# Kernel tuning notes

Hardware: AMD Instinct MI355X
Metric: run time of the kernel (lower is better)

## Reference

```python
import jax, jax.numpy as jnp
import numpy as np

# ---- module hyperparameters (from init_kwargs / tracker defaults) ----
D_MODEL = 512
D_HEAD = 512
LAMBDA_0 = 1.0        # A_0 = I / lambda_0
FIXED_LAMBDA = 1.0    # fixed penalty magnitude -> U = sqrt(lambda) * K (then / sqrt(d_head))
STAB_EPS = 1e-6       # InversePenaltyTracker.stabilization_eps
PERIODIC_EPS = 1e-6   # InversePenaltyTracker.periodic_eps
PERIOD = 128          # InversePenaltyTracker.period (periodic re-regularization)
EXPLODE_EPS = 1e-5    # fallback_add_explode coefficient
NORM_THRESH = 1000.0  # explosion detection threshold on Frobenius norms


def setup_inputs() -> dict:
    key = jax.random.key(0)
    ks = jax.random.split(key, 9)
    B, T, d = 8, 2048, D_MODEL
    s = 1.0 / np.sqrt(d)
    f32 = jnp.float32
    return {
        "x": jax.random.normal(ks[0], (B, T, d), f32),
        "Wq": (jax.random.normal(ks[1], (D_HEAD, d), f32) * s),
        "bq": jax.random.normal(ks[2], (D_HEAD,), f32) * 0.02,
        "Wk": (jax.random.normal(ks[3], (D_HEAD, d), f32) * s),
        "bk": jax.random.normal(ks[4], (D_HEAD,), f32) * 0.02,
        "Wv": (jax.random.normal(ks[5], (D_HEAD, d), f32) * s),
        "bv": jax.random.normal(ks[6], (D_HEAD,), f32) * 0.02,
        "Wo": (jax.random.normal(ks[7], (d, D_HEAD), f32) * s),
        "bo": jax.random.normal(ks[8], (d,), f32) * 0.02,
    }


def _vla_forward(x, Wq, bq, Wk, bk, Wv, bv, Wo, bo):
    B, T, _ = x.shape
    d = D_HEAD
    # projections (nn.Linear: x @ W.T + b)
    Q = jnp.einsum('btd,hd->bth', x, Wq) + bq
    K = jnp.einsum('btd,hd->bth', x, Wk) + bk
    V = jnp.einsum('btd,hd->bth', x, Wv) + bv

    # PenaltyBuilder (rank 1, fixed lambda): u_t = sqrt(lambda) * k_t, then / sqrt(d_head)
    U = (jnp.sqrt(jnp.float32(FIXED_LAMBDA)) / jnp.sqrt(jnp.float32(d))) * K
    s_seq = jnp.sum(K * Q, axis=-1)                                   # (B,T)
    Vn = V / (jnp.linalg.norm(V, axis=-1, keepdims=True) + 1e-6)      # (B,T,d)

    I = jnp.eye(d, dtype=jnp.float32)
    A0 = jnp.zeros((B, d, d), jnp.float32) + I / LAMBDA_0
    S0 = jnp.zeros((B, d, d), jnp.float32)

    def step(carry, inp):
        A, S = carry
        q, u, s_t, vn, t = inp  # q,u,vn: (B,d); s_t: (B,); t: scalar int
        # Sherman-Morrison rank-1 inverse update with stabilization
        z = jnp.einsum('bij,bj->bi', A, u)
        dot = jnp.sum(u * z, axis=-1)
        delta = jnp.maximum(1.0 + dot, 1e-6)
        unstable = (jnp.abs(delta) < STAB_EPS) | ~jnp.isfinite(delta)
        safe = jnp.where(unstable, 1.0, delta)
        upd = (z[:, :, None] * z[:, None, :]) / safe[:, None, None]
        A = jnp.where(unstable[:, None, None], A + STAB_EPS * I, A - upd)
        # periodic re-regularization (inv_step = t+1)
        A = jnp.where(((t + 1) % PERIOD) == 0, A + PERIODIC_EPS * I, A)
        # alpha_t = s_t * (A u_t)
        z2 = jnp.einsum('bij,bj->bi', A, u)
        alpha = s_t[:, None] * z2
        # memory update S += v_norm alpha^T
        S = S + vn[:, :, None] * alpha[:, None, :]
        # explosion guard
        Sn = jnp.linalg.norm(S.reshape(S.shape[0], -1), axis=-1)
        An = jnp.linalg.norm(A.reshape(A.shape[0], -1), axis=-1)
        A = jnp.where(((Sn > NORM_THRESH) | (An > NORM_THRESH))[:, None, None],
                      A + EXPLODE_EPS * I, A)
        o = jnp.einsum('bij,bj->bi', S, q)
        return (A, S), o

    xs = (jnp.swapaxes(Q, 0, 1), jnp.swapaxes(U, 0, 1),
          jnp.swapaxes(s_seq, 0, 1), jnp.swapaxes(Vn, 0, 1),
          jnp.arange(T))
    _, O = jax.lax.scan(step, (A0, S0), xs)    # O: (T,B,d)
    O = jnp.swapaxes(O, 0, 1)                  # (B,T,d)
    return jnp.einsum('bth,dh->btd', O, Wo) + bo


def reference(x, Wq, bq, Wk, bk, Wv, bv, Wo, bo):
    return _vla_forward(x, Wq, bq, Wk, bk, Wv, bv, Wo, bo)
```

## Files before the change

### kernel.cpp

```cpp
#include <hip/hip_runtime.h>
#include <hip/hip_bf16.h>

#define BB 8
#define TT 2048
#define DD 512
#define LL 128
#define NC 16
#define ETH 512

typedef unsigned short u16;
typedef unsigned int u32;
typedef __attribute__((ext_vector_type(8))) short bf16x8v;
typedef __attribute__((ext_vector_type(4))) float f32x4v;

__device__ __forceinline__ float bf2f(u32 h) { return __uint_as_float(h << 16); }
__device__ __forceinline__ u16 f2bf(float f) {
    u32 u = __float_as_uint(f);
    u += 0x7fffu + ((u >> 16) & 1u);
    return (u16)(u >> 16);
}
__device__ __forceinline__ float wred64(float v) {
    #pragma unroll
    for (int off = 32; off; off >>= 1) v += __shfl_xor(v, off);
    return v;
// ... 113 lines not shown
                        af[mf][ks], bfr[nf][ks], acc[mf][nf], 0, 0, 0);
    }
    const int l15 = lane & 15, lhi = lane >> 4;
    #pragma unroll
    for (int mf = 0; mf < 4; ++mf) {
        #pragma unroll
        for (int nf = 0; nf < 4; ++nf) {
            const int n = n0 + wn * 64 + nf * 16 + l15;
            const float bsv = bias[n];
            #pragma unroll
            for (int r = 0; r < 4; ++r) {
                const int m = m0 + wm * 64 + mf * 16 + lhi * 4 + r;
                const float val = (acc[mf][nf][r] + bsv) * outscale;
                if (OUT_BF) ((u16*)Cout)[(size_t)m * 512 + n] = f2bf(val);
                else        ((float*)Cout)[(size_t)m * 512 + n] = val;
            }
        }
    }
}

__device__ __forceinline__ void mfk6_body(const u16* __restrict__ Sb,
    const u16* __restrict__ Qt, const u16* __restrict__ AlT,
    const u16* __restrict__ Vnt, float* __restrict__ OBSA,
    float* __restrict__ dsum, const int bz)
{
    __shared__ u16 Ah[128 * 64];
    __shared__ u16 Bh[128 * 64];
    const int tid = threadIdx.x, wave = tid >> 6, lane = tid & 63;
    const int wm = wave >> 1, wn = wave & 1;
    const int m0 = blockIdx.x * 128, n0 = blockIdx.y * 128;

    f32x4v acc[4][4];
    #pragma unroll
    for (int i = 0; i < 4; ++i)
        #pragma unroll
        for (int j = 0; j < 4; ++j)
            acc[i][j] = (f32x4v){0.f, 0.f, 0.f, 0.f};

    const u16* Abase = Sb + (size_t)bz * 262144;
    const u16* Bbase = (n0 == 0) ? (Qt + (size_t)bz * 1048576)
                                 : (AlT + (size_t)bz * 65536);
    const u16* gA[4]; const u16* gB[4];
    #pragma unroll
    for (int i = 0; i < 4; ++i) {
        const int idx = i * 256 + tid, row = idx >> 3, c = idx & 7;
        const int kb = c ^ (row & 7);
        gA[i] = Abase + (size_t)(m0 + row) * 512 + kb * 8;
        gB[i] = Bbase + (size_t)row * 512 + kb * 8;
    }
    for (int k0 = 0; k0 < 512; k0 += 64) {
        __syncthreads();
        #pragma unroll
        for (int i = 0; i < 4; ++i) {
// ... 51 lines not shown
            }
        }
    if (n0 == 128) {
        const u16* Vn = Vnt + (size_t)bz * 1048576;
        #pragma unroll
        for (int nf = 0; nf < 4; ++nf) {
            const int n = n0 + wn * 64 + nf * 16 + l15;
            const int i2 = n - 128;
            float part = 0.f;
            #pragma unroll
            for (int mf = 0; mf < 4; ++mf) {
                const int m = m0 + wm * 64 + mf * 16 + lhi * 4;
                const ushort4 vr = *(const ushort4*)(Vn + (size_t)i2 * 512 + m);
                part += bf2f(vr.x) * acc[mf][nf][0] + bf2f(vr.y) * acc[mf][nf][1]
                      + bf2f(vr.z) * acc[mf][nf][2] + bf2f(vr.w) * acc[mf][nf][3];
            }
            part += __shfl_xor(part, 16);
            part += __shfl_xor(part, 32);
            if (lhi == 0) atomicAdd(dsum + bz * 128 + i2, part);
        }
    }
}

__global__ __launch_bounds__(256)
void mfk1_kernel(const u16* __restrict__ Abf, const u16* __restrict__ Ut,
                 float* __restrict__ Wm)
{
    __shared__ u16 Ah[128 * 64];
    __shared__ u16 Bh[128 * 64];
    const int tid = threadIdx.x, wave = tid >> 6, lane = tid & 63;
    const int wm = wave >> 1, wn = wave & 1;
    const int m0 = blockIdx.x * 128;
    const int bz = blockIdx.z;

    f32x4v acc[4][4];
    #pragma unroll
    for (int i = 0; i < 4; ++i)
        #pragma unroll
        for (int j = 0; j < 4; ++j)
            acc[i][j] = (f32x4v){0.f, 0.f, 0.f, 0.f};

    const u16* Abase = Abf + (size_t)bz * 262144;
    const u16* Bbase = Ut + (size_t)bz * 1048576;
    const u16* gA[4]; const u16* gB[4];
    #pragma unroll
    for (int i = 0; i < 4; ++i) {
        const int idx = i * 256 + tid, row = idx >> 3, c = idx & 7;
        const int kb = c ^ (row & 7);
        gA[i] = Abase + (size_t)(m0 + row) * 512 + kb * 8;
        gB[i] = Bbase + (size_t)row * 512 + kb * 8;
    }
    for (int k0 = 0; k0 < 512; k0 += 64) {
        __syncthreads();
        #pragma unroll
        for (int i = 0; i < 4; ++i) {
            const int dst = (i * 256 + wave * 64) * 8;
            __builtin_amdgcn_global_load_lds(
                (__attribute__((address_space(1))) void*)(gA[i] + k0),
                (__attribute__((address_space(3))) void*)(Ah + dst), 16, 0, 0);
            __builtin_amdgcn_global_load_lds(
                (__attribute__((address_space(1))) void*)(gB[i] + k0),
                (__attribute__((address_space(3))) void*)(Bh + dst), 16, 0, 0);
        }
        asm volatile("s_waitcnt vmcnt(0)" ::: "memory");
        __syncthreads();

        const int l15 = lane & 15, lhi = lane >> 4;
        bf16x8v af[4][2], bfr[4][2];
        #pragma unroll
        for (int mf = 0; mf < 4; ++mf) {
            const int row = wm * 64 + mf * 16 + l15, sw = (row & 7) << 4;
            #pragma unroll
            for (int ks = 0; ks < 2; ++ks) {
                const int kb2 = (ks * 64 + lhi * 16) ^ sw;
                af[mf][ks] = *(const bf16x8v*)((const char*)Ah + row * 128 + kb2);
            }
        }
        #pragma unroll
        for (int nf = 0; nf < 4; ++nf) {
            const int row = wn * 64 + nf * 16 + l15, sw = (row & 7) << 4;
            #pragma unroll
            for (int ks = 0; ks < 2; ++ks) {
                const int kb2 = (ks * 64 + lhi * 16) ^ sw;
                bfr[nf][ks] = *(const bf16x8v*)((const char*)Bh + row * 128 + kb2);
            }
        }
        #pragma unroll
        for (int ks = 0; ks < 2; ++ks)
            #pragma unroll
            for (int mf = 0; mf < 4; ++mf)
                #pragma unroll
                for (int nf = 0; nf < 4; ++nf)
                    acc[mf][nf] = __builtin_amdgcn_mfma_f32_16x16x32_bf16(
                        af[mf][ks], bfr[nf][ks], acc[mf][nf], 0, 0, 0);
    }
    const int l15 = lane & 15, lhi = lane >> 4;
    float* C = Wm + (size_t)bz * 65536;
    #pragma unroll
    for (int mf = 0; mf < 4; ++mf)
        #pragma unroll
        for (int nf = 0; nf < 4; ++nf) {
            const int n = wn * 64 + nf * 16 + l15;
            #pragma unroll
            for (int r = 0; r < 4; ++r) {
                const int m = m0 + wm * 64 + mf * 16 + lhi * 4 + r;
                C[(size_t)m * 128 + n] = acc[mf][nf][r];
            }
        }
}

__global__ __launch_bounds__(256)
void prep_kernel(const u16* __restrict__ Qb, const u16* __restrict__ Ub,
                 u16* __restrict__ Vb, float* __restrict__ sseq)
{
    const int lane = threadIdx.x & 63, wid = threadIdx.x >> 6;
    const int row = blockIdx.x * 4 + wid;
    const size_t base = (size_t)row * DD;
    const uint4 qr = *(const uint4*)(Qb + base + lane * 8);
    const uint4 ur = *(const uint4*)(Ub + base + lane * 8);
    const uint4 vr = *(const uint4*)(Vb + base + lane * 8);
    float q[8], u[8], v[8];
    unpack8(qr, q); unpack8(ur, u); unpack8(vr, v);
    float sd = 0.f, nv = 0.f;
    #pragma unroll
    for (int e = 0; e < 8; ++e) { sd = fmaf(q[e], u[e], sd); nv = fmaf(v[e], v[e], nv); }
    #pragma unroll
    for (int off = 32; off; off >>= 1) { sd += __shfl_xor(sd, off); nv += __shfl_xor(nv, off); }
    if (lane == 0) sseq[row] = sd * 22.627416997969522f;
    const float inv = 1.f / (sqrtf(nv) + 1e-6f);
    uint4 o;
    o.x = (u32)f2bf(v[0] * inv) | ((u32)f2bf(v[1] * inv) << 16);
// ... 15 lines not shown
        const int e0 = idx << 2;
        const int r = (e0 >> 9) & 511;
        const int c = e0 & 511;
        float4 v;
        v.x = (c + 0 == r) ? 1.f : 0.f;
        v.y = (c + 1 == r) ? 1.f : 0.f;
        v.z = (c + 2 == r) ? 1.f : 0.f;
        v.w = (c + 3 == r) ? 1.f : 0.f;
        A4[idx] = v;
        S4[idx] = make_float4(0.f, 0.f, 0.f, 0.f);
        Sbf4[idx] = z4;
        if (Abf4) {
            ushort4 a;
            a.x = (c + 0 == r) ? 0x3F80 : 0;
            a.y = (c + 1 == r) ? 0x3F80 : 0;
            a.z = (c + 2 == r) ? 0x3F80 : 0;
            a.w = (c + 3 == r) ? 0x3F80 : 0;
            Abf4[idx] = a;
        }
    }
    if (gtid < BB) { SnSq[gtid] = 0.f; AnAcc[gtid] = 512.f; }
}

struct GP {
    int alay, blay, epi;
    const void* Ap; const void* Bp;
    void* Cp; float* Cio;
    const float* gdiag; float* anacc;
    const float* invdp; const float* cap; const float* cbp;
    const u16* Ulastp; float* Zsp; float* Alphap;
    u16* albt; u16* sbf; u16* abf;
    int lda, ldb, ldc, K;
    long sA, sB, sC, sCio;
};

__device__ __forceinline__ void gemm_body(const GP& p, const int bz) {
    __shared__ __align__(16) float As[32][68];
    __shared__ __align__(16) float Bs[32][68];
    const int m0 = blockIdx.x * 64, n0 = blockIdx.y * 64;
    const int tid = threadIdx.x, tx = tid & 15, ty = tid >> 4;
    float acc[4][4] = {};
    for (int k0 = 0; k0 < p.K; k0 += 32) {
        if (p.alay == 0) {
            const float* A = (const float*)p.Ap + (size_t)bz * p.sA;
            #pragma unroll
            for (int h = 0; h < 2; ++h) {
// ... 135 lines not shown
            const int n = nb + j;
            const float iv = p.invdp[bz * 128 + n];
            const float cav = p.cap[bz * 128 + n];
            const float cbv = p.cbp[bz * 128 + n];
            #pragma unroll
            for (int i = 0; i < 4; ++i) {
                const int m = mb + i;
                const float z = acc[i][j];
                const size_t o = (size_t)m * 128 + n;
                Zb[o] = z;
                Zsb[o] = z * iv;
                float a = z * cav;
                if (cbv != 0.f) a = fmaf(cbv, bf2f(p.Ulastp[(size_t)bz * 1048576 + m]), a);
                Apb[o] = a;
                p.albt[(size_t)bz * 65536 + (size_t)n * 512 + m] = f2bf(a);
            }
        }
    }
}

__global__ __launch_bounds__(256) void gemmx(GP p) { gemm_body(p, blockIdx.z); }

__global__ __launch_bounds__(256)
void lvl5_kernel(const u16* Sb, const u16* AlT, const float* Alpha,
                 const u16* Qt, const u16* Vnt,
                 float* P, float* Ga, float* Gv, float* OBSA, float* dsum)
{
    const int z = blockIdx.z;
    if (z < 8) {
        mfk6_body(Sb, Qt, AlT, Vnt, OBSA, dsum, z);
        return;
    }
    if (blockIdx.x >= 2 || blockIdx.y >= 2) return;
    const int zz = z - 8, b = zz / 3, j = zz - b * 3;
    GP p{};
    p.K = 512; p.epi = 0; p.ldc = 128; p.sC = 16384;
    if (j == 0) {
        p.alay = 1; p.Ap = Alpha; p.lda = 128; p.sA = 65536;
        p.blay = 3; p.Bp = Qt; p.ldb = 512; p.sB = 1048576; p.Cp = P;
    } else if (j == 1) {
        p.alay = 1; p.Ap = Alpha; p.lda = 128; p.sA = 65536;
        p.blay = 0; p.Bp = Alpha; p.ldb = 128; p.sB = 65536; p.Cp = Ga;
    } else {
        p.alay = 2; p.Ap = Vnt; p.lda = 512; p.sA = 1048576;
        p.blay = 3; p.Bp = Vnt; p.ldb = 512; p.sB = 1048576; p.Cp = Gv;
    }
    gemm_body(p, b);
}

__global__ __launch_bounds__(256)
void lvl7_kernel(const float* P, const u16* Vnt, u16* Obt, const float* OBSA,
                 const float* Alpha, const float* Zs, const float* Z,
                 float* S, u16* Sbf, float* A, u16* Abf,
                 const float* gdiag, float* AnAcc)
{
    const int z = blockIdx.z;
    GP p{};
    if (z < 8) {
        p.alay = 0; p.Ap = Zs; p.lda = 128; p.sA = 65536;
        p.blay = 1; p.Bp = Z; p.ldb = 128; p.sB = 65536;
        p.epi = 1; p.Cio = A; p.sCio = 262144; p.ldc = 512;
        p.gdiag = gdiag; p.anacc = AnAcc; p.abf = Abf; p.K = 128;
        gemm_body(p, z);
    } else if (z < 16) {
        p.alay = 3; p.Ap = Vnt; p.lda = 512; p.sA = 1048576;
        p.blay = 1; p.Bp = Alpha; p.ldb = 128; p.sB = 65536;
        p.epi = 2; p.Cio = S; p.sbf = Sbf; p.sCio = 262144; p.ldc = 512; p.K = 128;
        gemm_body(p, z - 8);
    } else {
        if (blockIdx.x >= 2) return;
        p.alay = 4; p.Ap = P; p.lda = 128; p.sA = 16384;
        p.blay = 2; p.Bp = Vnt; p.ldb = 512; p.sB = 1048576;
        p.epi = 3; p.Cp = Obt; p.ldc = 512; p.sC = 1048576;
        p.Cio = (float*)OBSA; p.sCio = 131072; p.K = 128;
        gemm_body(p, z - 16);
    }
}

__global__ __launch_bounds__(512)
void elim_kernel(const float* __restrict__ G, float* __restrict__ Tg,
                 const float* __restrict__ sseq, float* __restrict__ invd,
                 float* __restrict__ ca, float* __restrict__ cb,
                 float* __restrict__ dsum_g, const int t0)
{
    const int b = blockIdx.x, tid = threadIdx.x, lane = tid & 63, wave = tid >> 6;
    __shared__ __align__(16) float E[128][132];
    __shared__ __align__(16) float Cs[128][132];
    __shared__ __align__(16) float Scr[2368];
    __shared__ float del[128];
    float (*Tm)[132] = E;
    float (*LpT)[132] = (float(*)[132])Scr;
    float (*SpT)[132] = (float(*)[132])(Scr + 1056);

    {
        const float4* Gb = (const float4*)(G + (size_t)b * 16384);
        for (int idx = tid; idx < 4096; idx += ETH) {
            const int r = idx >> 5, c4 = idx & 31;
            ((float4*)&E[r][0])[c4] = Gb[idx];
        }
    }
    if (tid < 128) dsum_g[b * 128 + tid] = 0.f;
    __syncthreads();

    for (int p = 0; p < 16; ++p) {
        const int pc0 = p * 8;
        if (wave == 0) {
            float pr0[8], pr1[8];
            #pragma unroll
            for (int j = 0; j < 8; ++j) {
                pr0[j] = E[pc0 + j][lane];
                pr1[j] = E[pc0 + j][64 + lane];
            }
            float dl[8];
            const bool hi = (pc0 >= 64);
            #pragma unroll
            for (int j = 0; j < 8; ++j) {
                const int t = pc0 + j;
                const int pl = t & 63;
                float prow[8];
                #pragma unroll
                for (int c = 0; c < 8; ++c) {
                    const float v0 = __shfl(pr0[c], pl);
                    const float v1 = __shfl(pr1[c], pl);
                    prow[c] = hi ? v1 : v0;
                }
                const float d = fmaxf(1.f + prow[j], 1e-6f);
                dl[j] = d;
                const float inv = 1.f / d;
                if (lane > t) {
                    const float coef = pr0[j] * inv;
                    #pragma unroll
                    for (int c = j + 1; c < 8; ++c) pr0[c] = fmaf(-coef, prow[c], pr0[c]);
                }
                if (lane + 64 > t) {
                    const float coef = pr1[j] * inv;
                    #pragma unroll
                    for (int c = j + 1; c < 8; ++c) pr1[c] = fmaf(-coef, prow[c], pr1[c]);
                }
            }
            #pragma unroll
            for (int j = 0; j < 8; ++j) {
                const float idj = 1.f / dl[j];
                const int t = pc0 + j;
                {
                    const bool below = (lane > t);
                    const float y = below ? pr0[j] : 0.f;
                    const float l = y * idj;
                    LpT[j][lane] = l; SpT[j][lane] = y; Cs[t][lane] = l;
                }
                {
                    const int r = lane + 64;
                    const bool below = (r > t);
                    const float y = below ? pr1[j] : 0.f;
                    const float l = y * idj;
                    LpT[j][r] = l; SpT[j][r] = y; Cs[t][r] = l;
                }
            }
            if (lane < 8) del[pc0 + lane] = dl[lane];
        }
        __syncthreads();
        const int r0b = pc0 + 8;
        if (r0b < 128) {
            const int nrows = 128 - r0b;
            const int c40 = r0b >> 2, nc4 = 32 - c40;
            for (int idx = tid; idx < nrows * nc4; idx += ETH) {
                const int rr = idx / nc4, cc = idx - rr * nc4;
                const int r = r0b + rr, c4 = c40 + cc;
                float4 e = ((float4*)&E[r][0])[c4];
                #pragma unroll
                for (int j = 0; j < 8; ++j) {
                    const float lv = LpT[j][r];
                    const float4 sv = ((const float4*)&SpT[j][0])[c4];
                    e.x = fmaf(-lv, sv.x, e.x);
                    e.y = fmaf(-lv, sv.y, e.y);
                    e.z = fmaf(-lv, sv.z, e.z);
                    e.w = fmaf(-lv, sv.w, e.w);
                }
                ((float4*)&E[r][0])[c4] = e;
            }
        }
        __syncthreads();
    }

    for (int idx = tid; idx < 4224; idx += ETH)
        ((float4*)&Tm[0][0])[idx] = make_float4(0.f, 0.f, 0.f, 0.f);
    __syncthreads();
    if (tid < 128) Tm[tid][tid] = 1.f;
    __syncthreads();
    {
        const int g = tid >> 3, c = tid & 7;
        if (g < 16) {
            for (int r2 = c - 1; r2 >= 0; --r2) {
                float s = 0.f;
                for (int kk = r2 + 1; kk <= c; ++kk)
                    s = fmaf(Cs[8 * g + r2][8 * g + kk],
                             (kk == c) ? 1.f : Tm[8 * g + kk][8 * g + c], s);
                Tm[8 * g + r2][8 * g + c] = -s;
            }
        }
    }
    __syncthreads();
    for (int s = 8; s <= 64; s <<= 1) {
        const int npairs = 64 / s;
        const int nj = (s == 64) ? 32 : s;
        const int stride = nj + 4;
        const int nj4 = nj >> 2;
        const int Nel = npairs * s * nj4;
        const int nhalf = (s == 64) ? 2 : 1;
        for (int jh = 0; jh < nhalf; ++jh) {
            for (int idx = tid; idx < Nel; idx += ETH) {
                const int p2 = idx / (s * nj4), rem = idx - p2 * s * nj4;
                const int i = rem / nj4, j4 = rem - i * nj4;
                const int I0 = 2 * s * p2, J0 = I0 + s;
                const int jc = j4 * 4 + jh * 32;
                float4 x = make_float4(0.f, 0.f, 0.f, 0.f);
                for (int k = 0; k < s; ++k) {
                    const float cv = Cs[I0 + i][J0 + k];
                    const float4 tv = *(const float4*)&Tm[J0 + k][J0 + jc];
                    x.x = fmaf(cv, tv.x, x.x);
                    x.y = fmaf(cv, tv.y, x.y);
                    x.z = fmaf(cv, tv.z, x.z);
                    x.w = fmaf(cv, tv.w, x.w);
                }
                *(float4*)&Scr[p2 * s * stride + i * stride + j4 * 4] = x;
            }
            __syncthreads();
            for (int idx = tid; idx < Nel; idx += ETH) {
                const int p2 = idx / (s * nj4), rem = idx - p2 * s * nj4;
                const int i = rem / nj4, j4 = rem - i * nj4;
                const int I0 = 2 * s * p2, J0 = I0 + s;
                const int jc = j4 * 4 + jh * 32;
                float4 y = make_float4(0.f, 0.f, 0.f, 0.f);
                for (int k = 0; k < s; ++k) {
                    const float tv = Tm[I0 + i][I0 + k];
                    const float4 xv = *(const float4*)&Scr[p2 * s * stride + k * stride + j4 * 4];
                    y.x = fmaf(tv, xv.x, y.x);
                    y.y = fmaf(tv, xv.y, y.y);
                    y.z = fmaf(tv, xv.z, y.z);
                    y.w = fmaf(tv, xv.w, y.w);
                }
                float4 o;
                o.x = -y.x; o.y = -y.y; o.z = -y.z; o.w = -y.w;
                *(float4*)&Tm[I0 + i][J0 + jc] = o;
            }
            __syncthreads();
        }
    }
    {
        float4* Tgb = (float4*)(Tg + (size_t)b * 16384);
        for (int idx = tid; idx < 4096; idx += ETH) {
            const int r = idx >> 5, c4 = idx & 31;
            Tgb[idx] = ((const float4*)&Tm[r][0])[c4];
        }
    }
    if (tid < 128) {
        const float d = del[tid];
        const float s = sseq[(size_t)b * TT + t0 + tid];
        invd[b * 128 + tid] = 1.f / d;
        ca[b * 128 + tid] = s / d;
        cb[b * 128 + tid] = (tid == 127) ? s * 1e-6f : 0.f;
    }
}

__global__ __launch_bounds__(256)
void guard_kernel(const float* __restrict__ dsum_g, const float* __restrict__ Ga,
                  const float* __restrict__ Gv, float* __restrict__ SnSq,
                  float* __restrict__ AnAcc, float* __restrict__ gdiag)
{
    const int b = blockIdx.x, tid = threadIdx.x;
    __shared__ float rpart[256], dsh[128], mdia[128];
    const int t = tid & 127, half = tid >> 7;
    const float* gv = Gv + (size_t)b * 16384 + t * 128;
    const float* ga = Ga + (size_t)b * 16384 + t * 128;
    float rs = 0.f;
    for (int j = half; j < t; j += 2) rs = fmaf(gv[j], ga[j], rs);
    rpart[tid] = rs;
    if (half == 0) { dsh[t] = dsum_g[b * 128 + t]; mdia[t] = gv[t] * ga[t]; }
    __syncthreads();
    if (tid == 0) {
        const float An2 = AnAcc[b];
        float Sn2 = SnSq[b], D = 0.f, T = 0.f;
        int ng = 0;
        for (int t2 = 0; t2 < 128; ++t2) {
// ... 37 lines not shown
    float* OBSA = (float*)(ws + (88ull << 20));
    float* G    = (float*)(ws + (92ull << 20));
    float* Tg   = (float*)(ws + (92ull << 20) + (512ull << 10));
    float* P    = (float*)(ws + (93ull << 20));
    float* Ga   = (float*)(ws + (93ull << 20) + (512ull << 10));
    float* Gv   = (float*)(ws + (94ull << 20));
    float* invd = (float*)(ws + (94ull << 20) + (512ull << 10));
    float* ca   = (float*)(ws + (94ull << 20) + (516ull << 10));
    float* cb   = (float*)(ws + (94ull << 20) + (520ull << 10));
    float* sseq = (float*)(ws + (94ull << 20) + (528ull << 10));
    float* SnSq = (float*)(ws + (94ull << 20) + (600ull << 10));
    float* AnAcc= (float*)(ws + (94ull << 20) + (600ull << 10) + 64);
    float* gdiag= (float*)(ws + (94ull << 20) + (600ull << 10) + 128);
    float* dsum = (float*)(ws + (94ull << 20) + (604ull << 10));
    u16* Wq_bf = (u16*)(ws + (95ull << 20));
    u16* Wk_bf = (u16*)(ws + (95ull << 20) + (512ull << 10));
    u16* Wv_bf = (u16*)(ws + (96ull << 20));
    u16* Wo_bf = (u16*)(ws + (96ull << 20) + (512ull << 10));
    u16* S_bf  = (u16*)(ws + (97ull << 20));
    u16* AlT   = (u16*)(ws + (101ull << 20));

    const bool big = (ws_size >= (111ull << 20));
    u16* A_bf = big ? (u16*)(ws + (102ull << 20)) : (u16*)nullptr;

    f2bf_kernel<<<2048, 256, 0, stream>>>((const float4*)x, (ushort4*)x_bf, 2097152);
    wconv_kernel<<<dim3(256, 4), 256, 0, stream>>>(
        (const float4*)Wq, (const float4*)Wk, (const float4*)Wv, (const float4*)Wo,
        (ushort4*)Wq_bf, (ushort4*)Wk_bf, (ushort4*)Wv_bf, (ushort4*)Wo_bf);

    mfma_gemm<1><<<dim3(128, 4), 256, 0, stream>>>(x_bf, Wq_bf, bq, Qb, 1.f);
    mfma_gemm<1><<<dim3(128, 4), 256, 0, stream>>>(x_bf, Wk_bf, bk, Ub, 0.04419417382415922f);
    mfma_gemm<1><<<dim3(128, 4), 256, 0, stream>>>(x_bf, Wv_bf, bv, Vnb, 1.f);
    prep_kernel<<<4096, 256, 0, stream>>>(Qb, Ub, Vnb, sseq);
    init_kernel<<<2048, 256, 0, stream>>>((float4*)A, (float4*)S, (ushort4*)S_bf,
                                          (ushort4*)A_bf, SnSq, AnAcc);

    for (int c = 0; c < NC; ++c) {
        const int t0 = c * LL;
        const u16* Ut = Ub + (size_t)t0 * 512;
        const u16* Qt = Qb + (size_t)t0 * 512;
        const u16* Vt = Vnb + (size_t)t0 * 512;
        if (big) {
            mfk1_kernel<<<dim3(4, 1, 8), 256, 0, stream>>>(A_bf, Ut, Wm);
        } else {
            GP p1{}; p1.alay = 0; p1.Ap = A; p1.lda = 512; p1.sA = 262144;
            p1.blay = 3; p1.Bp = Ut; p1.ldb = 512; p1.sB = 1048576;
            p1.epi = 0; p1.Cp = Wm; p1.ldc = 128; p1.sC = 65536; p1.K = 512;
            gemmx<<<dim3(8, 2, 8), 256, 0, stream>>>(p1);
        }
        GP p2{}; p2.alay = 2; p2.Ap = Ut; p2.lda = 512; p2.sA = 1048576;
        p2.blay = 0; p2.Bp = Wm; p2.ldb = 128; p2.sB = 65536;
        p2.epi = 0; p2.Cp = G; p2.ldc = 128; p2.sC = 16384; p2.K = 512;
        gemmx<<<dim3(2, 2, 8), 256, 0, stream>>>(p2);
        elim_kernel<<<8, 512, 0, stream>>>(G, Tg, sseq, invd, ca, cb, dsum, t0);
        GP p4{}; p4.alay = 0; p4.Ap = Wm; p4.lda = 128; p4.sA = 65536;
        p4.blay = 0; p4.Bp = Tg; p4.ldb = 128; p4.sB = 16384;
        p4.epi = 4; p4.Cp = Z; p4.Zsp = Zs; p4.Alphap = Alpha; p4.albt = AlT;
        p4.invdp = invd; p4.cap = ca; p4.cbp = cb;
        p4.Ulastp = Ub + (size_t)(t0 + 127) * 512;
        p4.K = 128; p4.ldc = 128; p4.sC = 65536;
        gemmx<<<dim3(8, 2, 8), 256, 0, stream>>>(p4);
        lvl5_kernel<<<dim3(4, 2, 32), 256, 0, stream>>>(S_bf, AlT, Alpha, Qt, Vt,
            P, Ga, Gv, OBSA, dsum);
        guard_kernel<<<8, 256, 0, stream>>>(dsum, Ga, Gv, SnSq, AnAcc, gdiag);
        lvl7_kernel<<<dim3(8, 8, 24), 256, 0, stream>>>(P, Vt, Ob + (size_t)t0 * 512, OBSA,
            Alpha, Zs, Z, S, S_bf, A, A_bf, gdiag, AnAcc);
    }
    mfma_gemm<0><<<dim3(128, 4), 256, 0, stream>>>(Ob, Wo_bf, bo, d_out, 1.f);
}
```

Before: 3.366 ms.

## Split elimination kernel and co-schedule independent S·Q and Vn Gram work

The monolithic per-batch elimination kernel is split into an LDL factor stage and a separate triangular-inverse kernel. The factor stage is packed into one launch together with work that does not depend on it: the S·Q product (mfk6q8 body) and the Vn Gram matrix (gv512), previously done in the later lvl5 launch, are moved earlier. This lets the serial 8-block factorization share the GPU with other blocks and shrinks lvl5's grid. The cost is an extra launch per chunk, a global round trip for the factor matrix, and many idle blocks that exit early in the combined grid.

```diff
diff --git a/kernel.cpp b/kernel.cpp
--- a/kernel.cpp
+++ b/kernel.cpp
@@ -159,13 +159,12 @@
 __device__ __forceinline__ void mfk6_body(const u16* __restrict__ Sb,
     const u16* __restrict__ Qt, const u16* __restrict__ AlT,
     const u16* __restrict__ Vnt, float* __restrict__ OBSA,
-    float* __restrict__ dsum, const int bz)
+    float* __restrict__ dsum, const int m0, const int n0, const int bz)
 {
     __shared__ u16 Ah[128 * 64];
     __shared__ u16 Bh[128 * 64];
     const int tid = threadIdx.x, wave = tid >> 6, lane = tid & 63;
     const int wm = wave >> 1, wn = wave & 1;
-    const int m0 = blockIdx.x * 128, n0 = blockIdx.y * 128;
 
     f32x4v acc[4][4];
     #pragma unroll
@@ -263,30 +262,29 @@
     }
 }
 
-__global__ __launch_bounds__(256)
-void mfk1_kernel(const u16* __restrict__ Abf, const u16* __restrict__ Ut,
-                 float* __restrict__ Wm)
-{
-    __shared__ u16 Ah[128 * 64];
-    __shared__ u16 Bh[128 * 64];
+__device__ __forceinline__ void mfk6q8_body(char* smemc,
+    const u16* __restrict__ Sb, const u16* __restrict__ Qt,
+    float* __restrict__ OBSA, const int bz)
+{
+    u16* Ah = (u16*)smemc;
+    u16* Bh = (u16*)(smemc + 16384);
     const int tid = threadIdx.x, wave = tid >> 6, lane = tid & 63;
     const int wm = wave >> 1, wn = wave & 1;
     const int m0 = blockIdx.x * 128;
-    const int bz = blockIdx.z;
-
-    f32x4v acc[4][4];
-    #pragma unroll
-    for (int i = 0; i < 4; ++i)
+
+    f32x4v acc[2][4];
+    #pragma unroll
+    for (int i = 0; i < 2; ++i)
         #pragma unroll
         for (int j = 0; j < 4; ++j)
             acc[i][j] = (f32x4v){0.f, 0.f, 0.f, 0.f};
 
-    const u16* Abase = Abf + (size_t)bz * 262144;
-    const u16* Bbase = Ut + (size_t)bz * 1048576;
-    const u16* gA[4]; const u16* gB[4];
-    #pragma unroll
-    for (int i = 0; i < 4; ++i) {
-        const int idx = i * 256 + tid, row = idx >> 3, c = idx & 7;
+    const u16* Abase = Sb + (size_t)bz * 262144;
+    const u16* Bbase = Qt + (size_t)bz * 1048576;
+    const u16* gA[2]; const u16* gB[2];
+    #pragma unroll
+    for (int i = 0; i < 2; ++i) {
+        const int idx = i * 512 + tid, row = idx >> 3, c = idx & 7;
         const int kb = c ^ (row & 7);
         gA[i] = Abase + (size_t)(m0 + row) * 512 + kb * 8;
         gB[i] = Bbase + (size_t)row * 512 + kb * 8;
@@ -294,8 +292,8 @@
     for (int k0 = 0; k0 < 512; k0 += 64) {
         __syncthreads();
         #pragma unroll
-        for (int i = 0; i < 4; ++i) {
-            const int dst = (i * 256 + wave * 64) * 8;
+        for (int i = 0; i < 2; ++i) {
+            const int dst = (i * 512 + wave * 64) * 8;
             __builtin_amdgcn_global_load_lds(
                 (__attribute__((address_space(1))) void*)(gA[i] + k0),
                 (__attribute__((address_space(3))) void*)(Ah + dst), 16, 0, 0);
@@ -307,10 +305,10 @@
         __syncthreads();
 
         const int l15 = lane & 15, lhi = lane >> 4;
-        bf16x8v af[4][2], bfr[4][2];
-        #pragma unroll
-        for (int mf = 0; mf < 4; ++mf) {
-            const int row = wm * 64 + mf * 16 + l15, sw = (row & 7) << 4;
+        bf16x8v af[2][2], bfr[4][2];
+        #pragma unroll
+        for (int mf = 0; mf < 2; ++mf) {
+            const int row = wm * 32 + mf * 16 + l15, sw = (row & 7) << 4;
             #pragma unroll
             for (int ks = 0; ks < 2; ++ks) {
                 const int kb2 = (ks * 64 + lhi * 16) ^ sw;
@@ -329,25 +327,282 @@
         #pragma unroll
         for (int ks = 0; ks < 2; ++ks)
             #pragma unroll
-            for (int mf = 0; mf < 4; ++mf)
+            for (int mf = 0; mf < 2; ++mf)
                 #pragma unroll
                 for (int nf = 0; nf < 4; ++nf)
                     acc[mf][nf] = __builtin_amdgcn_mfma_f32_16x16x32_bf16(
                         af[mf][ks], bfr[nf][ks], acc[mf][nf], 0, 0, 0);
     }
     const int l15 = lane & 15, lhi = lane >> 4;
-    float* C = Wm + (size_t)bz * 65536;
-    #pragma unroll
-    for (int mf = 0; mf < 4; ++mf)
+    float* C = OBSA + (size_t)bz * 131072;
+    #pragma unroll
+    for (int mf = 0; mf < 2; ++mf)
         #pragma unroll
         for (int nf = 0; nf < 4; ++nf) {
             const int n = wn * 64 + nf * 16 + l15;
             #pragma unroll
             for (int r = 0; r < 4; ++r) {
-                const int m = m0 + wm * 64 + mf * 16 + lhi * 4 + r;
-                C[(size_t)m * 128 + n] = acc[mf][nf][r];
-            }
-        }
+                const int m = m0 + wm * 32 + mf * 16 + lhi * 4 + r;
+                C[(size_t)m * 256 + n] = acc[mf][nf][r];
+            }
+        }
+}
+
+__device__ __forceinline__ void gv512_body(char* smemc, const u16* __restrict__ Vnt,
+    float* __restrict__ Gv, const int b)
+{
+    float (*As)[68] = (float(*)[68])smemc;
+    float (*Bs)[68] = (float(*)[68])(smemc + 8704);
+    const int tid = threadIdx.x;
+    const int m0 = blockIdx.x * 64, n0 = blockIdx.y * 64;
+    const u16* Vn = Vnt + (size_t)b * 1048576;
+    const int tx = tid & 15, ty = tid >> 4;
+    float acc[2][4] = {};
+    for (int k0 = 0; k0 < 512; k0 += 32) {
+        const int m = tid >> 3, k4 = (tid & 7) * 4;
+        const ushort4 ra = *(const ushort4*)(Vn + (size_t)(m0 + m) * 512 + k0 + k4);
+        As[k4][m]=bf2f(ra.x); As[k4+1][m]=bf2f(ra.y); As[k4+2][m]=bf2f(ra.z); As[k4+3][m]=bf2f(ra.w);
+        const ushort4 rb = *(const ushort4*)(Vn + (size_t)(n0 + m) * 512 + k0 + k4);
+        Bs[k4][m]=bf2f(rb.x); Bs[k4+1][m]=bf2f(rb.y); Bs[k4+2][m]=bf2f(rb.z); Bs[k4+3][m]=bf2f(rb.w);
+        __syncthreads();
+        #pragma unroll
+        for (int kk = 0; kk < 32; ++kk) {
+            const float a0 = As[kk][ty * 2], a1 = As[kk][ty * 2 + 1];
+            const float4 bv = *(const float4*)&Bs[kk][tx * 4];
+            acc[0][0] = fmaf(a0, bv.x, acc[0][0]);
+            acc[0][1] = fmaf(a0, bv.y, acc[0][1]);
+            acc[0][2] = fmaf(a0, bv.z, acc[0][2]);
+            acc[0][3] = fmaf(a0, bv.w, acc[0][3]);
+            acc[1][0] = fmaf(a1, bv.x, acc[1][0]);
+            acc[1][1] = fmaf(a1, bv.y, acc[1][1]);
+            acc[1][2] = fmaf(a1, bv.z, acc[1][2]);
+            acc[1][3] = fmaf(a1, bv.w, acc[1][3]);
+        }
+        __syncthreads();
+    }
+    float* G = Gv + (size_t)b * 16384;
+    #pragma unroll
+    for (int i = 0; i < 2; ++i)
+        #pragma unroll
+        for (int j = 0; j < 4; ++j)
+            G[(size_t)(m0 + ty * 2 + i) * 128 + n0 + tx * 4 + j] = acc[i][j];
+}
+
+__device__ __forceinline__ void factor_body(char* smemc,
+    const float* __restrict__ G, float* __restrict__ Cg,
+    const float* __restrict__ sseq, float* __restrict__ invd,
+    float* __restrict__ ca, float* __restrict__ cb, const int t0, const int b)
+{
+    const int tid = threadIdx.x, lane = tid & 63, wave = tid >> 6;
+    float (*E)[132]   = (float(*)[132])smemc;
+    float (*LpT)[132] = (float(*)[132])(smemc + 67584);
+    float (*SpT)[132] = (float(*)[132])(smemc + 71808);
+    float* del        = (float*)(smemc + 76032);
+
+    {
+        const float4* Gb = (const float4*)(G + (size_t)b * 16384);
+        for (int idx = tid; idx < 4096; idx += ETH) {
+            const int r = idx >> 5, c4 = idx & 31;
+            ((float4*)&E[r][0])[c4] = Gb[idx];
+        }
+    }
+    __syncthreads();
+    float* Cb = Cg + (size_t)b * 16384;
+
+    for (int p = 0; p < 16; ++p) {
+        const int pc0 = p * 8;
+        if (wave == 0) {
+            float pr0[8], pr1[8];
+            #pragma unroll
+            for (int j = 0; j < 8; ++j) {
+                pr0[j] = E[pc0 + j][lane];
+                pr1[j] = E[pc0 + j][64 + lane];
+            }
+            float dl[8];
+            const bool hi = (pc0 >= 64);
+            #pragma unroll
+            for (int j = 0; j < 8; ++j) {
+                const int t = pc0 + j;
+                const int pl = t & 63;
+                float prow[8];
+                if (hi) {
+                    #pragma unroll
+                    for (int c = 0; c < 8; ++c) prow[c] = __shfl(pr1[c], pl);
+                } else {
+                    #pragma unroll
+                    for (int c = 0; c < 8; ++c) prow[c] = __shfl(pr0[c], pl);
+                }
+                const float d = fmaxf(1.f + prow[j], 1e-6f);
+                dl[j] = d;
+                const float inv = 1.f / d;
+                if (lane > t) {
+                    const float coef = pr0[j] * inv;
+                    #pragma unroll
+                    for (int c = j + 1; c < 8; ++c) pr0[c] = fmaf(-coef, prow[c], pr0[c]);
+                }
+                if (lane + 64 > t) {
+                    const float coef = pr1[j] * inv;
+                    #pragma unroll
+                    for (int c = j + 1; c < 8; ++c) pr1[c] = fmaf(-coef, prow[c], pr1[c]);
+                }
+            }
+            #pragma unroll
+            for (int j = 0; j < 8; ++j) {
+                const float idj = 1.f / dl[j];
+                const int t = pc0 + j;
+                {
+                    const bool below = (lane > t);
+                    const float y = below ? pr0[j] : 0.f;
+                    const float l = y * idj;
+                    LpT[j][lane] = l; SpT[j][lane] = y;
+                    Cb[(size_t)t * 128 + lane] = l;
+                }
+                {
+                    const int r = lane + 64;
+                    const bool below = (r > t);
+                    const float y = below ? pr1[j] : 0.f;
+                    const float l = y * idj;
+                    LpT[j][r] = l; SpT[j][r] = y;
+                    Cb[(size_t)t * 128 + r] = l;
+                }
+            }
+            if (lane < 8) del[pc0 + lane] = dl[lane];
+        }
+        __syncthreads();
+        const int r0b = pc0 + 8;
+        if (r0b < 128) {
+            const int nrows = 128 - r0b;
+            const int c40 = r0b >> 2, nc4 = 32 - c40;
+            for (int idx = tid; idx < nrows * nc4; idx += ETH) {
+                const int rr = idx / nc4, cc = idx - rr * nc4;
+                const int r = r0b + rr, c4 = c40 + cc;
+                float4 e = ((float4*)&E[r][0])[c4];
+                #pragma unroll
+                for (int j = 0; j < 8; ++j) {
+                    const float lv = LpT[j][r];
+                    const float4 sv = ((const float4*)&SpT[j][0])[c4];
+                    e.x = fmaf(-lv, sv.x, e.x);
+                    e.y = fmaf(-lv, sv.y, e.y);
+                    e.z = fmaf(-lv, sv.z, e.z);
+                    e.w = fmaf(-lv, sv.w, e.w);
+                }
+                ((float4*)&E[r][0])[c4] = e;
+            }
+        }
+        __syncthreads();
+    }
+    if (tid < 128) {
+        const float d = del[tid];
+        const float s = sseq[(size_t)b * TT + t0 + tid];
+        invd[b * 128 + tid] = 1.f / d;
+        ca[b * 128 + tid] = s / d;
+        cb[b * 128 + tid] = (tid == 127) ? s * 1e-6f : 0.f;
+    }
+}
+
+__global__ __launch_bounds__(512)
+void lvl3_kernel(const float* __restrict__ G, float* __restrict__ Cg,
+                 const float* __restrict__ sseq, float* __restrict__ invd,
+                 float* __restrict__ ca, float* __restrict__ cb,
+                 const u16* __restrict__ Vnt, const u16* __restrict__ Sb,
+                 const u16* __restrict__ Qt, float* __restrict__ Gv,
+                 float* __restrict__ OBSA, const int t0)
+{
+    __shared__ __align__(16) char smem[76800];
+    const int z = blockIdx.z;
+    if (z >= 16) {
+        if (blockIdx.y != 0) return;
+        mfk6q8_body(smem, Sb, Qt, OBSA, z - 16);
+        return;
+    }
+    if (z >= 8) {
+        if (blockIdx.x >= 2 || blockIdx.y >= 2) return;
+        gv512_body(smem, Vnt, Gv, z - 8);
+        return;
+    }
+    if (blockIdx.x != 0 || blockIdx.y != 0) return;
+    factor_body(smem, G, Cg, sseq, invd, ca, cb, t0, z);
+}
+
+__global__ __launch_bounds__(512)
+void inv_kernel(const float* __restrict__ Cg, float* __restrict__ Tg)
+{
+    const int b = blockIdx.x, tid = threadIdx.x;
+    __shared__ __align__(16) float Tm[128][132];
+    __shared__ __align__(16) float Scr[2368];
+    const float* Cb = Cg + (size_t)b * 16384;
+
+    for (int idx = tid; idx < 4224; idx += ETH)
+        ((float4*)&Tm[0][0])[idx] = make_float4(0.f, 0.f, 0.f, 0.f);
+    __syncthreads();
+    if (tid < 128) Tm[tid][tid] = 1.f;
+    __syncthreads();
+    {
+        const int g = tid >> 3, c = tid & 7;
+        if (g < 16) {
+            for (int r2 = c - 1; r2 >= 0; --r2) {
+                float s = 0.f;
+                for (int kk = r2 + 1; kk <= c; ++kk)
+                    s = fmaf(Cb[(size_t)(8 * g + r2) * 128 + 8 * g + kk],
+                             (kk == c) ? 1.f : Tm[8 * g + kk][8 * g + c], s);
+                Tm[8 * g + r2][8 * g + c] = -s;
+            }
+        }
+    }
+    __syncthreads();
+    for (int s = 8; s <= 64; s <<= 1) {
+        const int npairs = 64 / s;
+        const int nj = (s == 64) ? 32 : s;
+        const int stride = nj + 4;
+        const int nj4 = nj >> 2;
+        const int Nel = npairs * s * nj4;
+        const int nhalf = (s == 64) ? 2 : 1;
+        for (int jh = 0; jh < nhalf; ++jh) {
+            for (int idx = tid; idx < Nel; idx += ETH) {
+                const int p2 = idx / (s * nj4), rem = idx - p2 * s * nj4;
+                const int i = rem / nj4, j4 = rem - i * nj4;
+                const int I0 = 2 * s * p2, J0 = I0 + s;
+                const int jc = j4 * 4 + jh * 32;
+                float4 x = make_float4(0.f, 0.f, 0.f, 0.f);
+                for (int k = 0; k < s; ++k) {
+                    const float cv = Cb[(size_t)(I0 + i) * 128 + J0 + k];
+                    const float4 tv = *(const float4*)&Tm[J0 + k][J0 + jc];
+                    x.x = fmaf(cv, tv.x, x.x);
+                    x.y = fmaf(cv, tv.y, x.y);
+                    x.z = fmaf(cv, tv.z, x.z);
+                    x.w = fmaf(cv, tv.w, x.w);
+                }
+                *(float4*)&Scr[p2 * s * stride + i * stride + j4 * 4] = x;
+            }
+            __syncthreads();
+            for (int idx = tid; idx < Nel; idx += ETH) {
+                const int p2 = idx / (s * nj4), rem = idx - p2 * s * nj4;
+                const int i = rem / nj4, j4 = rem - i * nj4;
+                const int I0 = 2 * s * p2, J0 = I0 + s;
+                const int jc = j4 * 4 + jh * 32;
+                float4 y = make_float4(0.f, 0.f, 0.f, 0.f);
+                for (int k = 0; k < s; ++k) {
+                    const float tv = Tm[I0 + i][I0 + k];
+                    const float4 xv = *(const float4*)&Scr[p2 * s * stride + k * stride + j4 * 4];
+                    y.x = fmaf(tv, xv.x, y.x);
+                    y.y = fmaf(tv, xv.y, y.y);
+                    y.z = fmaf(tv, xv.z, y.z);
+                    y.w = fmaf(tv, xv.w, y.w);
+                }
+                float4 o;
+                o.x = -y.x; o.y = -y.y; o.z = -y.z; o.w = -y.w;
+                *(float4*)&Tm[I0 + i][J0 + jc] = o;
+            }
+            __syncthreads();
+        }
+    }
+    {
+        float4* Tgb = (float4*)(Tg + (size_t)b * 16384);
+        for (int idx = tid; idx < 4096; idx += ETH) {
+            const int r = idx >> 5, c4 = idx & 31;
+            Tgb[idx] = ((const float4*)&Tm[r][0])[c4];
+        }
+    }
 }
 
 __global__ __launch_bounds__(256)
@@ -409,6 +664,93 @@
     if (gtid < BB) { SnSq[gtid] = 0.f; AnAcc[gtid] = 512.f; }
 }
 
+__global__ __launch_bounds__(256)
+void mfk1_kernel(const u16* __restrict__ Abf, const u16* __restrict__ Ut,
+                 float* __restrict__ Wm)
+{
+    __shared__ u16 Ah[128 * 64];
+    __shared__ u16 Bh[128 * 64];
+    const int tid = threadIdx.x, wave = tid >> 6, lane = tid & 63;
+    const int wm = wave >> 1, wn = wave & 1;
+    const int m0 = blockIdx.x * 128;
+    const int bz = blockIdx.z;
+
+    f32x4v acc[4][4];
+    #pragma unroll
+    for (int i = 0; i < 4; ++i)
+        #pragma unroll
+        for (int j = 0; j < 4; ++j)
+            acc[i][j] = (f32x4v){0.f, 0.f, 0.f, 0.f};
+
+    const u16* Abase = Abf + (size_t)bz * 262144;
+    const u16* Bbase = Ut + (size_t)bz * 1048576;
+    const u16* gA[4]; const u16* gB[4];
+    #pragma unroll
+    for (int i = 0; i < 4; ++i) {
+        const int idx = i * 256 + tid, row = idx >> 3, c = idx & 7;
+        const int kb = c ^ (row & 7);
+        gA[i] = Abase + (size_t)(m0 + row) * 512 + kb * 8;
+        gB[i] = Bbase + (size_t)row * 512 + kb * 8;
+    }
+    for (int k0 = 0; k0 < 512; k0 += 64) {
+        __syncthreads();
+        #pragma unroll
+        for (int i = 0; i < 4; ++i) {
+            const int dst = (i * 256 + wave * 64) * 8;
+            __builtin_amdgcn_global_load_lds(
+                (__attribute__((address_space(1))) void*)(gA[i] + k0),
+                (__attribute__((address_space(3))) void*)(Ah + dst), 16, 0, 0);
+            __builtin_amdgcn_global_load_lds(
+                (__attribute__((address_space(1))) void*)(gB[i] + k0),
+                (__attribute__((address_space(3))) void*)(Bh + dst), 16, 0, 0);
+        }
+        asm volatile("s_waitcnt vmcnt(0)" ::: "memory");
+        __syncthreads();
+
+        const int l15 = lane & 15, lhi = lane >> 4;
+        bf16x8v af[4][2], bfr[4][2];
+        #pragma unroll
+        for (int mf = 0; mf < 4; ++mf) {
+            const int row = wm * 64 + mf * 16 + l15, sw = (row & 7) << 4;
+            #pragma unroll
+            for (int ks = 0; ks < 2; ++ks) {
+                const int kb2 = (ks * 64 + lhi * 16) ^ sw;
+                af[mf][ks] = *(const bf16x8v*)((const char*)Ah + row * 128 + kb2);
+            }
+        }
+        #pragma unroll
+        for (int nf = 0; nf < 4; ++nf) {
+            const int row = wn * 64 + nf * 16 + l15, sw = (row & 7) << 4;
+            #pragma unroll
+            for (int ks = 0; ks < 2; ++ks) {
+                const int kb2 = (ks * 64 + lhi * 16) ^ sw;
+                bfr[nf][ks] = *(const bf16x8v*)((const char*)Bh + row * 128 + kb2);
+            }
+        }
+        #pragma unroll
+        for (int ks = 0; ks < 2; ++ks)
+            #pragma unroll
+            for (int mf = 0; mf < 4; ++mf)
+                #pragma unroll
+                for (int nf = 0; nf < 4; ++nf)
+                    acc[mf][nf] = __builtin_amdgcn_mfma_f32_16x16x32_bf16(
+                        af[mf][ks], bfr[nf][ks], acc[mf][nf], 0, 0, 0);
+    }
+    const int l15 = lane & 15, lhi = lane >> 4;
+    float* C = Wm + (size_t)bz * 65536;
+    #pragma unroll
+    for (int mf = 0; mf < 4; ++mf)
+        #pragma unroll
+        for (int nf = 0; nf < 4; ++nf) {
+            const int n = wn * 64 + nf * 16 + l15;
+            #pragma unroll
+            for (int r = 0; r < 4; ++r) {
+                const int m = m0 + wm * 64 + mf * 16 + lhi * 4 + r;
+                C[(size_t)m * 128 + n] = acc[mf][nf][r];
+            }
+        }
+}
+
 struct GP {
     int alay, blay, epi;
     const void* Ap; const void* Bp;
@@ -590,30 +932,36 @@
 __global__ __launch_bounds__(256) void gemmx(GP p) { gemm_body(p, blockIdx.z); }
 
 __global__ __launch_bounds__(256)
-void lvl5_kernel(const u16* Sb, const u16* AlT, const float* Alpha,
-                 const u16* Qt, const u16* Vnt,
-                 float* P, float* Ga, float* Gv, float* OBSA, float* dsum)
+void k2_kernel(GP p, float* __restrict__ dsum)
+{
+    if (blockIdx.x == 0 && blockIdx.y == 0 && threadIdx.x < 128)
+        dsum[blockIdx.z * 128 + threadIdx.x] = 0.f;
+    gemm_body(p, blockIdx.z);
+}
+
+__global__ __launch_bounds__(256)
+void lvl5c_kernel(const u16* Sb, const u16* AlT, const float* Alpha,
+                  const u16* Qt, const u16* Vnt,
+                  float* P, float* Ga, float* OBSA, float* dsum)
 {
     const int z = blockIdx.z;
     if (z < 8) {
-        mfk6_body(Sb, Qt, AlT, Vnt, OBSA, dsum, z);
+        if (blockIdx.y != 0) return;
+        mfk6_body(Sb, Qt, AlT, Vnt, OBSA, dsum, blockIdx.x * 128, 128, z);
         return;
     }
     if (blockIdx.x >= 2 || blockIdx.y >= 2) return;
-    const int zz = z - 8, b = zz / 3, j = zz - b * 3;
     GP p{};
     p.K = 512; p.epi = 0; p.ldc = 128; p.sC = 16384;
-    if (j == 0) {
+    if (z < 16) {
         p.alay = 1; p.Ap = Alpha; p.lda = 128; p.sA = 65536;
         p.blay = 3; p.Bp = Qt; p.ldb = 512; p.sB = 1048576; p.Cp = P;
-    } else if (j == 1) {
+        gemm_body(p, z - 8);
+    } else {
         p.alay = 1; p.Ap = Alpha; p.lda = 128; p.sA = 65536;
         p.blay = 0; p.Bp = Alpha; p.ldb = 128; p.sB = 65536; p.Cp = Ga;
-    } else {
-        p.alay = 2; p.Ap = Vnt; p.lda = 512; p.sA = 1048576;
-        p.blay = 3; p.Bp = Vnt; p.ldb = 512; p.sB = 1048576; p.Cp = Gv;
-    }
-    gemm_body(p, b);
+        gemm_body(p, z - 16);
+    }
 }
 
 __global__ __launch_bounds__(256)
@@ -642,191 +990,6 @@
         p.epi = 3; p.Cp = Obt; p.ldc = 512; p.sC = 1048576;
         p.Cio = (float*)OBSA; p.sCio = 131072; p.K = 128;
         gemm_body(p, z - 16);
-    }
-}
-
-__global__ __launch_bounds__(512)
-void elim_kernel(const float* __restrict__ G, float* __restrict__ Tg,
-                 const float* __restrict__ sseq, float* __restrict__ invd,
-                 float* __restrict__ ca, float* __restrict__ cb,
-                 float* __restrict__ dsum_g, const int t0)
-{
-    const int b = blockIdx.x, tid = threadIdx.x, lane = tid & 63, wave = tid >> 6;
-    __shared__ __align__(16) float E[128][132];
-    __shared__ __align__(16) float Cs[128][132];
-    __shared__ __align__(16) float Scr[2368];
-    __shared__ float del[128];
-    float (*Tm)[132] = E;
-    float (*LpT)[132] = (float(*)[132])Scr;
-    float (*SpT)[132] = (float(*)[132])(Scr + 1056);
-
-    {
-        const float4* Gb = (const float4*)(G + (size_t)b * 16384);
-        for (int idx = tid; idx < 4096; idx += ETH) {
-            const int r = idx >> 5, c4 = idx & 31;
-            ((float4*)&E[r][0])[c4] = Gb[idx];
-        }
-    }
-    if (tid < 128) dsum_g[b * 128 + tid] = 0.f;
-    __syncthreads();
-
-    for (int p = 0; p < 16; ++p) {
-        const int pc0 = p * 8;
-        if (wave == 0) {
-            float pr0[8], pr1[8];
-            #pragma unroll
-            for (int j = 0; j < 8; ++j) {
-                pr0[j] = E[pc0 + j][lane];
-                pr1[j] = E[pc0 + j][64 + lane];
-            }
-            float dl[8];
-            const bool hi = (pc0 >= 64);
-            #pragma unroll
-            for (int j = 0; j < 8; ++j) {
-                const int t = pc0 + j;
-                const int pl = t & 63;
-                float prow[8];
-                #pragma unroll
-                for (int c = 0; c < 8; ++c) {
-                    const float v0 = __shfl(pr0[c], pl);
-                    const float v1 = __shfl(pr1[c], pl);
-                    prow[c] = hi ? v1 : v0;
-                }
-                const float d = fmaxf(1.f + prow[j], 1e-6f);
-                dl[j] = d;
-                const float inv = 1.f / d;
-                if (lane > t) {
-                    const float coef = pr0[j] * inv;
-                    #pragma unroll
-                    for (int c = j + 1; c < 8; ++c) pr0[c] = fmaf(-coef, prow[c], pr0[c]);
-                }
-                if (lane + 64 > t) {
-                    const float coef = pr1[j] * inv;
-                    #pragma unroll
-                    for (int c = j + 1; c < 8; ++c) pr1[c] = fmaf(-coef, prow[c], pr1[c]);
-                }
-            }
-            #pragma unroll
-            for (int j = 0; j < 8; ++j) {
-                const float idj = 1.f / dl[j];
-                const int t = pc0 + j;
-                {
-                    const bool below = (lane > t);
-                    const float y = below ? pr0[j] : 0.f;
-                    const float l = y * idj;
-                    LpT[j][lane] = l; SpT[j][lane] = y; Cs[t][lane] = l;
-                }
-                {
-                    const int r = lane + 64;
-                    const bool below = (r > t);
-                    const float y = below ? pr1[j] : 0.f;
-                    const float l = y * idj;
-                    LpT[j][r] = l; SpT[j][r] = y; Cs[t][r] = l;
-                }
-            }
-            if (lane < 8) del[pc0 + lane] = dl[lane];
-        }
-        __syncthreads();
-        const int r0b = pc0 + 8;
-        if (r0b < 128) {
-            const int nrows = 128 - r0b;
-            const int c40 = r0b >> 2, nc4 = 32 - c40;
-            for (int idx = tid; idx < nrows * nc4; idx += ETH) {
-                const int rr = idx / nc4, cc = idx - rr * nc4;
-                const int r = r0b + rr, c4 = c40 + cc;
-                float4 e = ((float4*)&E[r][0])[c4];
-                #pragma unroll
-                for (int j = 0; j < 8; ++j) {
-                    const float lv = LpT[j][r];
-                    const float4 sv = ((const float4*)&SpT[j][0])[c4];
-                    e.x = fmaf(-lv, sv.x, e.x);
-                    e.y = fmaf(-lv, sv.y, e.y);
-                    e.z = fmaf(-lv, sv.z, e.z);
-                    e.w = fmaf(-lv, sv.w, e.w);
-                }
-                ((float4*)&E[r][0])[c4] = e;
-            }
-        }
-        __syncthreads();
-    }
-
-    for (int idx = tid; idx < 4224; idx += ETH)
-        ((float4*)&Tm[0][0])[idx] = make_float4(0.f, 0.f, 0.f, 0.f);
-    __syncthreads();
-    if (tid < 128) Tm[tid][tid] = 1.f;
-    __syncthreads();
-    {
-        const int g = tid >> 3, c = tid & 7;
-        if (g < 16) {
-            for (int r2 = c - 1; r2 >= 0; --r2) {
-                float s = 0.f;
-                for (int kk = r2 + 1; kk <= c; ++kk)
-                    s = fmaf(Cs[8 * g + r2][8 * g + kk],
-                             (kk == c) ? 1.f : Tm[8 * g + kk][8 * g + c], s);
-                Tm[8 * g + r2][8 * g + c] = -s;
-            }
-        }
-    }
-    __syncthreads();
-    for (int s = 8; s <= 64; s <<= 1) {
-        const int npairs = 64 / s;
-        const int nj = (s == 64) ? 32 : s;
-        const int stride = nj + 4;
-        const int nj4 = nj >> 2;
-        const int Nel = npairs * s * nj4;
-        const int nhalf = (s == 64) ? 2 : 1;
-        for (int jh = 0; jh < nhalf; ++jh) {
-            for (int idx = tid; idx < Nel; idx += ETH) {
-                const int p2 = idx / (s * nj4), rem = idx - p2 * s * nj4;
-                const int i = rem / nj4, j4 = rem - i * nj4;
-                const int I0 = 2 * s * p2, J0 = I0 + s;
-                const int jc = j4 * 4 + jh * 32;
-                float4 x = make_float4(0.f, 0.f, 0.f, 0.f);
-                for (int k = 0; k < s; ++k) {
-                    const float cv = Cs[I0 + i][J0 + k];
-                    const float4 tv = *(const float4*)&Tm[J0 + k][J0 + jc];
-                    x.x = fmaf(cv, tv.x, x.x);
-                    x.y = fmaf(cv, tv.y, x.y);
-                    x.z = fmaf(cv, tv.z, x.z);
-                    x.w = fmaf(cv, tv.w, x.w);
-                }
-                *(float4*)&Scr[p2 * s * stride + i * stride + j4 * 4] = x;
-            }
-            __syncthreads();
-            for (int idx = tid; idx < Nel; idx += ETH) {
-                const int p2 = idx / (s * nj4), rem = idx - p2 * s * nj4;
-                const int i = rem / nj4, j4 = rem - i * nj4;
-                const int I0 = 2 * s * p2, J0 = I0 + s;
-                const int jc = j4 * 4 + jh * 32;
-                float4 y = make_float4(0.f, 0.f, 0.f, 0.f);
-                for (int k = 0; k < s; ++k) {
-                    const float tv = Tm[I0 + i][I0 + k];
-                    const float4 xv = *(const float4*)&Scr[p2 * s * stride + k * stride + j4 * 4];
-                    y.x = fmaf(tv, xv.x, y.x);
-                    y.y = fmaf(tv, xv.y, y.y);
-                    y.z = fmaf(tv, xv.z, y.z);
-                    y.w = fmaf(tv, xv.w, y.w);
-                }
-                float4 o;
-                o.x = -y.x; o.y = -y.y; o.z = -y.z; o.w = -y.w;
-                *(float4*)&Tm[I0 + i][J0 + jc] = o;
-            }
-            __syncthreads();
-        }
-    }
-    {
-        float4* Tgb = (float4*)(Tg + (size_t)b * 16384);
-        for (int idx = tid; idx < 4096; idx += ETH) {
-            const int r = idx >> 5, c4 = idx & 31;
-            Tgb[idx] = ((const float4*)&Tm[r][0])[c4];
-        }
-    }
-    if (tid < 128) {
-        const float d = del[tid];
-        const float s = sseq[(size_t)b * TT + t0 + tid];
-        invd[b * 128 + tid] = 1.f / d;
-        ca[b * 128 + tid] = s / d;
-        cb[b * 128 + tid] = (tid == 127) ? s * 1e-6f : 0.f;
     }
 }
 
@@ -910,6 +1073,7 @@
 
     const bool big = (ws_size >= (111ull << 20));
     u16* A_bf = big ? (u16*)(ws + (102ull << 20)) : (u16*)nullptr;
+    float* Cg = big ? (float*)(ws + (110ull << 20)) : (float*)(ws + (102ull << 20));
 
     f2bf_kernel<<<2048, 256, 0, stream>>>((const float4*)x, (ushort4*)x_bf, 2097152);
     wconv_kernel<<<dim3(256, 4), 256, 0, stream>>>(
@@ -939,8 +1103,10 @@
         GP p2{}; p2.alay = 2; p2.Ap = Ut; p2.lda = 512; p2.sA = 1048576;
         p2.blay = 0; p2.Bp = Wm; p2.ldb = 128; p2.sB = 65536;
         p2.epi = 0; p2.Cp = G; p2.ldc = 128; p2.sC = 16384; p2.K = 512;
-        gemmx<<<dim3(2, 2, 8), 256, 0, stream>>>(p2);
-        elim_kernel<<<8, 512, 0, stream>>>(G, Tg, sseq, invd, ca, cb, dsum, t0);
+        k2_kernel<<<dim3(2, 2, 8), 256, 0, stream>>>(p2, dsum);
+        lvl3_kernel<<<dim3(4, 2, 24), 512, 0, stream>>>(G, Cg, sseq, invd, ca, cb,
+            Vt, S_bf, Qt, Gv, OBSA, t0);
+        inv_kernel<<<8, 512, 0, stream>>>(Cg, Tg);
         GP p4{}; p4.alay = 0; p4.Ap = Wm; p4.lda = 128; p4.sA = 65536;
         p4.blay = 0; p4.Bp = Tg; p4.ldb = 128; p4.sB = 16384;
         p4.epi = 4; p4.Cp = Z; p4.Zsp = Zs; p4.Alphap = Alpha; p4.albt = AlT;
@@ -948,8 +1114,8 @@
         p4.Ulastp = Ub + (size_t)(t0 + 127) * 512;
         p4.K = 128; p4.ldc = 128; p4.sC = 65536;
         gemmx<<<dim3(8, 2, 8), 256, 0, stream>>>(p4);
-        lvl5_kernel<<<dim3(4, 2, 32), 256, 0, stream>>>(S_bf, AlT, Alpha, Qt, Vt,
-            P, Ga, Gv, OBSA, dsum);
+        lvl5c_kernel<<<dim3(4, 2, 24), 256, 0, stream>>>(S_bf, AlT, Alpha, Qt, Vt,
+            P, Ga, OBSA, dsum);
         guard_kernel<<<8, 256, 0, stream>>>(dsum, Ga, Gv, SnSq, AnAcc, gdiag);
         lvl7_kernel<<<dim3(8, 8, 24), 256, 0, stream>>>(P, Vt, Ob + (size_t)t0 * 512, OBSA,
             Alpha, Zs, Z, S, S_bf, A, A_bf, gdiag, AnAcc);
```

After: 3.818 ms. 1.13x slower.
